# Kernel tuning notes

Measured on AMD Instinct MI355X. Metric: run time of the kernel, lower is better.

## Reference

```python
import jax, jax.numpy as jnp
import numpy as np

LN_EPS = 1e-9

def _layer_norm(x, g, b):
    mu = jnp.mean(x, axis=-1, keepdims=True)
    var = jnp.mean((x - mu) ** 2, axis=-1, keepdims=True)
    return (x - mu) * jax.lax.rsqrt(var + LN_EPS) * g + b

def _ffn(x, w1, b1, w2, b2, ln_g, ln_b):
    h = jax.nn.gelu(x @ w1 + b1, approximate=False)
    h = h @ w2 + b2
    return _layer_norm(h, ln_g, ln_b)

def _kernel_mean(x, y):
    d = x.shape[1]
    x2 = jnp.sum(x * x, axis=1)[:, None]
    y2 = jnp.sum(y * y, axis=1)[None, :]
    sq = x2 + y2 - 2.0 * (x @ y.T)  # [Nx, Ny]
    return jnp.mean(jnp.exp(-sq / (d * d)))

def _mmd(x, y):
    return _kernel_mean(x, x) + _kernel_mean(y, y) - 2.0 * _kernel_mean(x, y)

def setup_inputs() -> dict:
    key = jax.random.key(0)
    ks = jax.random.split(key, 8)
    B, S, D, DI, DL = 8, 512, 1024, 4096, 64
    s = lambda fan: 1.0 / np.sqrt(fan)
    return {
        "hidden": jax.random.normal(ks[0], (B, S, D), jnp.float32),
        "true_samples": jax.random.normal(ks[1], (B * S, DL), jnp.float32),
        "enc_w1": jax.random.normal(ks[2], (D, DI), jnp.float32) * s(D),
        "enc_b1": jnp.zeros((DI,), jnp.float32),
        "enc_w2": jax.random.normal(ks[3], (DI, DL), jnp.float32) * s(DI),
        "enc_b2": jnp.zeros((DL,), jnp.float32),
        "enc_ln_g": jnp.ones((DL,), jnp.float32),
        "enc_ln_b": jnp.zeros((DL,), jnp.float32),
        "dec_w1": jax.random.normal(ks[4], (DL, DI), jnp.float32) * s(DL),
        "dec_b1": jnp.zeros((DI,), jnp.float32),
        "dec_w2": jax.random.normal(ks[5], (DI, D), jnp.float32) * s(DI),
        "dec_b2": jnp.zeros((D,), jnp.float32),
        "dec_ln_g": jnp.ones((D,), jnp.float32),
        "dec_ln_b": jnp.zeros((D,), jnp.float32),
    }

def reference(hidden, true_samples, enc_w1, enc_b1, enc_w2, enc_b2, enc_ln_g, enc_ln_b,
              dec_w1, dec_b1, dec_w2, dec_b2, dec_ln_g, dec_ln_b):
    latent = _ffn(hidden, enc_w1, enc_b1, enc_w2, enc_b2, enc_ln_g, enc_ln_b)  # [B,S,DL]
    recon = _ffn(latent, dec_w1, dec_b1, dec_w2, dec_b2, dec_ln_g, dec_ln_b)   # [B,S,D]
    B, S, DL = latent.shape
    lat_flat = latent.reshape(-1, DL)  # [B*S, DL]
    reg_loss = _mmd(true_samples, lat_flat) / B * S
    return recon, latent, reg_loss
```

## Files before the change

### kernel.cpp

```cpp
#include <hip/hip_runtime.h>
#include <hip/hip_bf16.h>
#include <math.h>


typedef __attribute__((ext_vector_type(8))) short short8;
typedef __attribute__((ext_vector_type(4))) float float4a;
typedef __attribute__((ext_vector_type(4))) unsigned short us4;

__device__ inline ushort bf16r(float x) {
    union { float f; unsigned u; } c; c.f = x;
    unsigned r = (c.u + 0x7fffu + ((c.u >> 16) & 1u)) >> 16;
    return (ushort)r;
}

__device__ inline void gld_lds16(const void* g, void* l) {
    __builtin_amdgcn_global_load_lds(
        (const __attribute__((address_space(1))) void*)g,
        (__attribute__((address_space(3))) void*)l, 16, 0, 0);
}

template <int N> __device__ inline void wait_vmcnt() {
    if constexpr (N == 0) asm volatile("s_waitcnt vmcnt(0)" ::: "memory");
    else if constexpr (N == 4) asm volatile("s_waitcnt vmcnt(4)" ::: "memory");
    else if constexpr (N == 6) asm volatile("s_waitcnt vmcnt(6)" ::: "memory");
}

template <int N> __device__ inline void wait_lgkmcnt() {
    if constexpr (N == 0) asm volatile("s_waitcnt lgkmcnt(0)" ::: "memory");
    else if constexpr (N == 2) asm volatile("s_waitcnt lgkmcnt(2)" ::: "memory");
    else if constexpr (N == 4) asm volatile("s_waitcnt lgkmcnt(4)" ::: "memory");
    else if constexpr (N == 6) asm volatile("s_waitcnt lgkmcnt(6)" ::: "memory");
    else if constexpr (N == 8) asm volatile("s_waitcnt lgkmcnt(8)" ::: "memory");
    else if constexpr (N == 12) asm volatile("s_waitcnt lgkmcnt(12)" ::: "memory");
}

__device__ inline void wait_lgkm_dyn(int n) {
    if (n == 0) wait_lgkmcnt<0>();
    else if (n == 2) wait_lgkmcnt<2>();
    else if (n == 4) wait_lgkmcnt<4>();
    else if (n == 6) wait_lgkmcnt<6>();
    else wait_lgkmcnt<8>();
}

__device__ inline float fast_gelu(float v) {
    float v2 = v * v;
    float u = v * __builtin_fmaf(0.07135481627f, v2, 1.5957691216f);
    u = fminf(u, 30.0f);
    float e = __expf(u);
    return v * e * __builtin_amdgcn_rcpf(e + 1.0f);
}

__global__ __launch_bounds__(256) void k_pre(
        const float* __restrict__ hidden, ushort* __restrict__ A1bf,
        const float* __restrict__ tsamp, ushort* __restrict__ Tbf,
        float* __restrict__ sq_t, float* __restrict__ acc,
        const float* __restrict__ i0, ushort* __restrict__ o0,
        const float* __restrict__ i1, ushort* __restrict__ o1,
        const float* __restrict__ i2, ushort* __restrict__ o2,
        const float* __restrict__ i3, ushort* __restrict__ o3) {
    int b = blockIdx.x, tid = threadIdx.x;
    if (b == 0 && tid < 24) acc[tid] = 0.0f;
    if (b < 4096) {
        int i = b * 1024 + tid * 4;
        float4 v = *(const float4*)(hidden + i);
        us4 o = {bf16r(v.x), bf16r(v.y), bf16r(v.z), bf16r(v.w)};
        *(us4*)(A1bf + i) = o;
        return;
    }
    if (b < 4352) {
        int i = (b - 4096) * 1024 + tid * 4;
        float4 v = *(const float4*)(tsamp + i);
        us4 o = {bf16r(v.x), bf16r(v.y), bf16r(v.z), bf16r(v.w)};
        *(us4*)(Tbf + i) = o;
        float s = v.x * v.x + v.y * v.y + v.z * v.z + v.w * v.w;
#pragma unroll
        for (int off = 8; off; off >>= 1) s += __shfl_xor(s, off);
        if ((tid & 15) == 0) sq_t[i >> 6] = s;
        return;
    }
    __shared__ float t[32][65];
    const float* in; ushort* out; int R, C;
    int lb = b - 4352;
    if (lb < 2048)      { in = i0; out = o0; R = 1024; C = 4096; }
    else if (lb < 2176) { in = i1; out = o1; R = 4096; C = 64;   lb -= 2048; }
    else if (lb < 2304) { in = i2; out = o2; R = 64;   C = 4096; lb -= 2176; }
    else                { in = i3; out = o3; R = 4096; C = 1024; lb -= 2304; }
    int bx = (lb % (C / 32)) * 32;
    int by = (lb / (C / 32)) * 64;
    int tx = tid & 31, ty = tid >> 5;
#pragma unroll
    for (int i = 0; i < 64; i += 8)
        t[tx][i + ty] = in[(size_t)(by + i + ty) * C + (bx + tx)];
    __syncthreads();
#pragma unroll
    for (int i = 0; i < 32; i += 8) {
        int c = i + ty;
        ushort2 o;
        o.x = bf16r(t[c][2 * tx]);
        o.y = bf16r(t[c][2 * tx + 1]);
        *(ushort2*)(&out[(size_t)(bx + c) * R + by + 2 * tx]) = o;
    }
}

template <int BN, int EPI, bool SWZ>
__global__ __launch_bounds__(256) void k_gemm(
        const ushort* __restrict__ A, const ushort* __restrict__ Bt,
        const float* __restrict__ bias, void* __restrict__ Out,
        float* __restrict__ Out2, int M, int N, int K, int KC) {
    constexpr int BM = 128, BK = 64;
    constexpr int WAVES_N = BN / 64;
    constexpr int WAVES_M = 4 / WAVES_N;
    constexpr int WM = BM / WAVES_M;
    constexpr int MT = WM / 16;
    constexpr int NT = 4;
    constexpr int CA = BM / 32, CB = BN / 32;

    __shared__ ushort sA[BM * 64];
    __shared__ ushort sB[BN * 64];

    const int tid  = threadIdx.x;
    const int wave = tid >> 6, lane = tid & 63;
    const int wm = wave / WAVES_N, wn = wave % WAVES_N;
    int bx = blockIdx.x, by = blockIdx.y;
    if constexpr (SWZ) {
        int lin = blockIdx.x + gridDim.x * blockIdx.y;
        by = lin % gridDim.y;
        bx = lin / gridDim.y;
    }
    const int m0 = by * BM, n0 = bx * BN;
    const int lrow = lane & 15, lq = lane >> 4;
    const int srow8 = lane >> 3;
    const int sk8   = lane & 7;
    const int kbeg = blockIdx.z * KC;

    const ushort* pA[CA]; unsigned lA[CA];
#pragma unroll
    for (int j = 0; j < CA; ++j) {
        int c = wave * CA + j;
        int r = c * 8 + srow8;
        pA[j] = &A[(size_t)(m0 + r) * K + kbeg + ((sk8 ^ (r & 7)) * 8)];
        lA[j] = c * 512;
    }
    const ushort* pB[CB]; unsigned lB[CB];
#pragma unroll
    for (int j = 0; j < CB; ++j) {
        int c = wave * CB + j;
        int r = c * 8 + srow8;
        pB[j] = &Bt[(size_t)(n0 + r) * K + kbeg + ((sk8 ^ (r & 7)) * 8)];
        lB[j] = c * 512;
    }
    unsigned aoff[2][MT], boff[2][NT];
#pragma unroll
    for (int h = 0; h < 2; ++h) {
#pragma unroll
        for (int mt = 0; mt < MT; ++mt) {
            int r = wm * WM + mt * 16 + lrow;
            aoff[h][mt] = r * 64 + (((h * 4 + lq) ^ (r & 7)) * 8);
        }
#pragma unroll
        for (int nt = 0; nt < NT; ++nt) {
            int r = wn * 64 + nt * 16 + lrow;
            boff[h][nt] = r * 64 + (((h * 4 + lq) ^ (r & 7)) * 8);
        }
    }

    float4a acc[MT][NT];
#pragma unroll
    for (int mt = 0; mt < MT; ++mt)
#pragma unroll
        for (int nt = 0; nt < NT; ++nt)
            acc[mt][nt] = (float4a){0.f, 0.f, 0.f, 0.f};

    for (int k0 = 0; k0 < KC; k0 += BK) {
#pragma unroll
        for (int j = 0; j < CA; ++j) {
            gld_lds16(pA[j], &sA[lA[j]]);
            pA[j] += BK;
        }
#pragma unroll
        for (int j = 0; j < CB; ++j) {
            gld_lds16(pB[j], &sB[lB[j]]);
            pB[j] += BK;
        }
        __syncthreads();
#pragma unroll
        for (int h = 0; h < 2; ++h) {
            short8 af[MT], bfr[NT];
#pragma unroll
            for (int mt = 0; mt < MT; ++mt)
                af[mt] = *(short8*)(&sA[aoff[h][mt]]);
#pragma unroll
            for (int nt = 0; nt < NT; ++nt)
                bfr[nt] = *(short8*)(&sB[boff[h][nt]]);
#pragma unroll
            for (int mt = 0; mt < MT; ++mt)
#pragma unroll
                for (int nt = 0; nt < NT; ++nt)
                    acc[mt][nt] = __builtin_amdgcn_mfma_f32_16x16x32_bf16(
                        af[mt], bfr[nt], acc[mt][nt], 0, 0, 0);
        }
        __syncthreads();
    }

    float* dstp = nullptr;
    if constexpr (EPI == 2) {
        if (Out2 && blockIdx.z) dstp = Out2;
        else dstp = (float*)Out + (size_t)blockIdx.z * M * N;
    }
#pragma unroll
    for (int mt = 0; mt < MT; ++mt)
#pragma unroll
        for (int nt = 0; nt < NT; ++nt) {
            int col = n0 + wn * 64 + nt * 16 + lrow;
            float bv = 0.f;
            if constexpr (EPI != 2) bv = bias[col];
#pragma unroll
            for (int r = 0; r < 4; ++r) {
                int row = m0 + wm * WM + mt * 16 + lq * 4 + r;
                float v = acc[mt][nt][r] + bv;
                if constexpr (EPI == 0) {
                    ((ushort*)Out)[(size_t)row * N + col] = bf16r(fast_gelu(v));
                } else if constexpr (EPI == 1) {
                    ((float*)Out)[(size_t)row * N + col] = v;
                } else {
                    dstp[(size_t)row * N + col] = v;
                }
            }
        }
}

template <int BN, int EPI, int CX, int CY>
__global__ __launch_bounds__(512, 2) void k_gemm256mb(
        const ushort* __restrict__ A, const ushort* __restrict__ Bt,
        const float* __restrict__ bias, void* __restrict__ Out,
        float* __restrict__ Out2, int M, int N, int K, int KC) {
    constexpr int BM = 256, BK = 64;
    constexpr int AI = 4;
    constexpr int BI = BN / 64;
    constexpr int WAVES_N = BN / 64;
    constexpr int WAVES_M = 8 / WAVES_N;
    constexpr int WM = BM / WAVES_M;
    constexpr int MT = WM / 16;
    constexpr int NT = 4;

    __shared__ ushort sA[2][BM * 64];
    __shared__ ushort sB[2][BN * 64];

    const int tid = threadIdx.x;
    const int wave = tid >> 6, lane = tid & 63;
    const int wm = wave / WAVES_N, wn = wave % WAVES_N;

    const int gx = gridDim.x, gy = gridDim.y;
    const int lin = blockIdx.x + gx * (blockIdx.y + gy * blockIdx.z);
    const int nwg = gx * gy * gridDim.z;
    const int cpx = nwg >> 3;
    const int swz = (lin & 7) * cpx + (lin >> 3);
    const int nz  = gx * gy;
    const int zz  = swz / nz;
    const int rr  = swz % nz;
    const int chunk = rr / (CX * CY);
    const int lcl   = rr % (CX * CY);
    const int ncx   = gx / CX;
    const int bx = (chunk % ncx) * CX + (lcl % CX);
    const int by = (chunk / ncx) * CY + (lcl / CX);

    const int m0 = by * BM, n0 = bx * BN;
    const int lrow = lane & 15, lq = lane >> 4;
    const int kbeg = zz * KC;
    const int nT = KC / BK;

    const int crow = tid >> 3;
    const int ck8  = (tid & 7) ^ (crow & 7);
    const ushort* pAbase = A  + (size_t)(m0 + crow) * K + kbeg + ck8 * 8;
    const ushort* pBbase = Bt + (size_t)(n0 + crow) * K + kbeg + ck8 * 8;

    const int a0  = (wm * WM + lrow) * 64;
    const int b0  = (wn * 64 + lrow) * 64;
    const int sw0 = ((lq) ^ (lrow & 7)) * 8;
    const int sw1 = ((4 + lq) ^ (lrow & 7)) * 8;

    float4a acc[MT][NT];
#pragma unroll
    for (int mt = 0; mt < MT; ++mt)
#pragma unroll
        for (int nt = 0; nt < NT; ++nt)
            acc[mt][nt] = (float4a){0.f, 0.f, 0.f, 0.f};

#pragma unroll
    for (int j = 0; j < AI; ++j)
        gld_lds16(pAbase + (size_t)j * 64 * K, &sA[0][j * 4096 + wave * 512]);
#pragma unroll
    for (int j = 0; j < BI; ++j)
        gld_lds16(pBbase + (size_t)j * 64 * K, &sB[0][j * 4096 + wave * 512]);
    wait_vmcnt<0>();
    __builtin_amdgcn_s_barrier();
    __builtin_amdgcn_sched_barrier(0);

    for (int t = 0; t < nT; ++t) {
        const int d = t & 1;
        const bool pf1 = (t + 1 < nT);
        const size_t koff1 = (size_t)(t + 1) * BK;

        short8 af0[MT], bfr0[NT], af1[MT], bfr1[NT];
#pragma unroll
        for (int mt = 0; mt < MT; ++mt)
            af0[mt] = *(const short8*)(&sA[d][a0 + mt * 1024 + sw0]);
#pragma unroll
        for (int nt = 0; nt < NT; ++nt)
            bfr0[nt] = *(const short8*)(&sB[d][b0 + nt * 1024 + sw0]);
        __builtin_amdgcn_sched_barrier(0);
#pragma unroll
        for (int mt = 0; mt < MT; ++mt)
            af1[mt] = *(const short8*)(&sA[d][a0 + mt * 1024 + sw1]);
#pragma unroll
        for (int nt = 0; nt < NT; ++nt)
            bfr1[nt] = *(const short8*)(&sB[d][b0 + nt * 1024 + sw1]);
        if (pf1) {
#pragma unroll
            for (int j = 0; j < AI; ++j)
                gld_lds16(pAbase + (size_t)j * 64 * K + koff1,
                          &sA[d ^ 1][j * 4096 + wave * 512]);
#pragma unroll
            for (int j = 0; j < BI; ++j)
                gld_lds16(pBbase + (size_t)j * 64 * K + koff1,
                          &sB[d ^ 1][j * 4096 + wave * 512]);
        }
        wait_lgkmcnt<MT + 4>();
        __builtin_amdgcn_sched_barrier(0);
        __builtin_amdgcn_s_setprio(1);
#pragma unroll
        for (int mt = 0; mt < MT; ++mt)
#pragma unroll
            for (int nt = 0; nt < NT; ++nt)
                acc[mt][nt] = __builtin_amdgcn_mfma_f32_16x16x32_bf16(
                    af0[mt], bfr0[nt], acc[mt][nt], 0, 0, 0);
        __builtin_amdgcn_s_setprio(0);
        wait_lgkmcnt<0>();
        __builtin_amdgcn_sched_barrier(0);
        __builtin_amdgcn_s_setprio(1);
#pragma unroll
        for (int mt = 0; mt < MT; ++mt)
#pragma unroll
            for (int nt = 0; nt < NT; ++nt)
                acc[mt][nt] = __builtin_amdgcn_mfma_f32_16x16x32_bf16(
                    af1[mt], bfr1[nt], acc[mt][nt], 0, 0, 0);
        __builtin_amdgcn_s_setprio(0);
        if (pf1) {
            wait_vmcnt<0>();
            __builtin_amdgcn_s_barrier();
            __builtin_amdgcn_sched_barrier(0);
        }
    }

    float* dstp = nullptr;
    if constexpr (EPI == 2) {
        if (Out2 && zz) dstp = Out2;
        else dstp = (float*)Out + (size_t)zz * M * N;
    }
#pragma unroll
    for (int mt = 0; mt < MT; ++mt)
#pragma unroll
        for (int nt = 0; nt < NT; ++nt) {
            const int col = n0 + wn * 64 + nt * 16 + lrow;
            float bv = 0.f;
            if constexpr (EPI == 0) bv = bias[col];
#pragma unroll
            for (int r = 0; r < 4; ++r) {
                const int row = m0 + wm * WM + mt * 16 + lq * 4 + r;
                float v = acc[mt][nt][r] + bv;
                if constexpr (EPI == 0)
                    ((ushort*)Out)[(size_t)row * N + col] = bf16r(fast_gelu(v));
                else
                    dstp[(size_t)row * N + col] = v;
            }
        }
}

template <int BN, int EPI, int CX, int CY>
__global__ __launch_bounds__(512, 2) void k_gemm256sp(
        const ushort* __restrict__ A, const ushort* __restrict__ Bt,
        const float* __restrict__ bias, void* __restrict__ Out,
        float* __restrict__ Out2, int M, int N, int K, int KC) {
    constexpr int BM = 256, BK = 64;
    constexpr int AI = 4;
    constexpr int BI = BN / 64;
    constexpr int WAVES_N = BN / 64;
    constexpr int WAVES_M = 8 / WAVES_N;
    constexpr int WM = BM / WAVES_M;
    constexpr int MT = WM / 16;
    constexpr int NT = 4;
    constexpr int NS = MT;
    constexpr int NS2 = MT / 2;

    __shared__ ushort sA[2][BM * 64];
    __shared__ ushort sB[2][BN * 64];

    const int tid = threadIdx.x;
    const int wave = tid >> 6, lane = tid & 63;
    const int wm = wave / WAVES_N, wn = wave % WAVES_N;

    const int gx = gridDim.x, gy = gridDim.y;
    const int lin = blockIdx.x + gx * (blockIdx.y + gy * blockIdx.z);
    const int nwg = gx * gy * gridDim.z;
    const int cpx = nwg >> 3;
    const int swz = (lin & 7) * cpx + (lin >> 3);
    const int nz  = gx * gy;
    const int zz  = swz / nz;
    const int rr  = swz % nz;
    const int chunk = rr / (CX * CY);
    const int lcl   = rr % (CX * CY);
    const int ncx   = gx / CX;
    const int bx = (chunk % ncx) * CX + (lcl % CX);
    const int by = (chunk / ncx) * CY + (lcl / CX);

    const int m0 = by * BM, n0 = bx * BN;
    const int lrow = lane & 15, lq = lane >> 4;
    const int kbeg = zz * KC;
    const int nT = KC / BK;

    const int crow = tid >> 3;
    const int ck8  = (tid & 7) ^ (crow & 7);
    const ushort* pAbase = A  + (size_t)(m0 + crow) * K + kbeg + ck8 * 8;
    const ushort* pBbase = Bt + (size_t)(n0 + crow) * K + kbeg + ck8 * 8;

    const int a0  = (wm * WM + lrow) * 64;
    const int b0  = (wn * 64 + lrow) * 64;
    const int sw0 = ((lq) ^ (lrow & 7)) * 8;
    const int sw1 = ((4 + lq) ^ (lrow & 7)) * 8;

    float4a acc[MT][NT];
#pragma unroll
    for (int mt = 0; mt < MT; ++mt)
#pragma unroll
        for (int nt = 0; nt < NT; ++nt)
            acc[mt][nt] = (float4a){0.f, 0.f, 0.f, 0.f};

#pragma unroll
    for (int j = 0; j < AI; ++j)
        gld_lds16(pAbase + (size_t)j * 64 * K, &sA[0][j * 4096 + wave * 512]);
#pragma unroll
    for (int j = 0; j < BI; ++j)
        gld_lds16(pBbase + (size_t)j * 64 * K, &sB[0][j * 4096 + wave * 512]);
    wait_vmcnt<0>();
    __builtin_amdgcn_s_barrier();
    __builtin_amdgcn_sched_barrier(0);

    for (int t = 0; t < nT; ++t) {
        const int d = t & 1;
        const bool pf1 = (t + 1 < nT);
        const size_t koff1 = (size_t)(t + 1) * BK;

        short8 af[NS][2], bfr[2][NT];

#pragma unroll
        for (int nt = 0; nt < NT; ++nt)
            bfr[0][nt] = *(const short8*)(&sB[d][b0 + nt * 1024 + sw0]);
        af[0][0] = *(const short8*)(&sA[d][a0 + 0 * 1024 + sw0]);
        af[0][1] = *(const short8*)(&sA[d][a0 + 1 * 1024 + sw0]);
        __builtin_amdgcn_sched_barrier(0);
        af[1][0] = *(const short8*)(&sA[d][a0 + 2 * 1024 + sw0]);
        af[1][1] = *(const short8*)(&sA[d][a0 + 3 * 1024 + sw0]);
        __builtin_amdgcn_sched_barrier(0);
        if (pf1) {
#pragma unroll
            for (int j = 0; j < AI; ++j)
                gld_lds16(pAbase + (size_t)j * 64 * K + koff1,
                          &sA[d ^ 1][j * 4096 + wave * 512]);
#pragma unroll
            for (int j = 0; j < BI; ++j)
                gld_lds16(pBbase + (size_t)j * 64 * K + koff1,
                          &sB[d ^ 1][j * 4096 + wave * 512]);
        }
        __builtin_amdgcn_sched_barrier(0);

#pragma unroll
        for (int s = 0; s < NS; ++s) {
            const int s2 = s + 2;
            if (s2 < NS) {
                const int h2 = s2 / NS2;
                const int mb2 = (s2 % NS2) * 2;
                const int swh2 = h2 ? sw1 : sw0;
                if ((s2 % NS2) == 0) {
#pragma unroll
                    for (int nt = 0; nt < NT; ++nt)
                        bfr[h2][nt] =
                            *(const short8*)(&sB[d][b0 + nt * 1024 + swh2]);
                }
                af[s2][0] = *(const short8*)(&sA[d][a0 + (mb2 + 0) * 1024 + swh2]);
                af[s2][1] = *(const short8*)(&sA[d][a0 + (mb2 + 1) * 1024 + swh2]);
                __builtin_amdgcn_sched_barrier(0);
            }
            int Ns = 0;
            if (s + 1 < NS) Ns += (((s + 1) % NS2) == 0) ? (2 + NT) : 2;
            if (s + 2 < NS) Ns += (((s + 2) % NS2) == 0) ? (2 + NT) : 2;
            wait_lgkm_dyn(Ns);
            __builtin_amdgcn_sched_barrier(0);
            const int h = s / NS2, mb = (s % NS2) * 2;
            __builtin_amdgcn_s_setprio(1);
#pragma unroll
            for (int i = 0; i < 2; ++i)
#pragma unroll
                for (int nt = 0; nt < NT; ++nt)
                    acc[mb + i][nt] = __builtin_amdgcn_mfma_f32_16x16x32_bf16(
                        af[s][i], bfr[h][nt], acc[mb + i][nt], 0, 0, 0);
            __builtin_amdgcn_s_setprio(0);
        }
        if (pf1) {
            wait_vmcnt<0>();
            __builtin_amdgcn_s_barrier();
            __builtin_amdgcn_sched_barrier(0);
        }
    }

    float* dstp = nullptr;
    if constexpr (EPI == 2) {
        if (Out2 && zz) dstp = Out2;
        else dstp = (float*)Out + (size_t)zz * M * N;
    }
#pragma unroll
    for (int mt = 0; mt < MT; ++mt)
#pragma unroll
        for (int nt = 0; nt < NT; ++nt) {
            const int col = n0 + wn * 64 + nt * 16 + lrow;
            float bv = 0.f;
            if constexpr (EPI == 0) bv = bias[col];
#pragma unroll
            for (int r = 0; r < 4; ++r) {
                const int row = m0 + wm * WM + mt * 16 + lq * 4 + r;
                float v = acc[mt][nt][r] + bv;
                if constexpr (EPI == 0)
                    ((ushort*)Out)[(size_t)row * N + col] = bf16r(fast_gelu(v));
                else
                    dstp[(size_t)row * N + col] = v;
            }
        }
}

__global__ __launch_bounds__(256) void k_gram_all(
        const ushort* __restrict__ Tbf, const ushort* __restrict__ Lbf,
        const float* __restrict__ sq_t, const float* __restrict__ sq_l,
        float* __restrict__ accum) {
    __shared__ ushort sX[128 * 64];
    __shared__ ushort sY[128 * 64];
    __shared__ float red[4];

    int id = blockIdx.x;
    int pair, tbx, tby; float w;
    if (id < 1056) {
        pair = (id < 528) ? 0 : 1;
        int t = (pair == 0) ? id : id - 528;
        int r = (int)((sqrtf(8.0f * t + 1.0f) - 1.0f) * 0.5f);
        while ((r + 1) * (r + 2) / 2 <= t) ++r;
        while (r * (r + 1) / 2 > t) --r;
        tby = r; tbx = t - r * (r + 1) / 2;
        w = (tbx == tby) ? 1.0f : 2.0f;
    } else {
        pair = 2; int t = id - 1056;
        tbx = t & 31; tby = t >> 5; w = 1.0f;
    }
    const ushort* Xb = (pair == 1) ? Lbf : Tbf;
    const ushort* Yb = (pair == 0) ? Tbf : Lbf;
    const float* sqX = (pair == 1) ? sq_l : sq_t;
    const float* sqY = (pair == 0) ? sq_t : sq_l;

    const int tid  = threadIdx.x;
    const int wave = tid >> 6, lane = tid & 63;
    const int wm = wave >> 1, wn = wave & 1;
    const int bx = tbx * 128, by = tby * 128;
    const int lrow = lane & 15, lq = lane >> 4;
    const int srow8 = lane >> 3, sk8 = lane & 7;

#pragma unroll
    for (int j = 0; j < 4; ++j) {
        int c = wave * 4 + j;
        int r = c * 8 + srow8;
        int kc = (sk8 ^ (r & 7)) * 8;
        gld_lds16(&Xb[(size_t)(bx + r) * 64 + kc], &sX[c * 512]);
        gld_lds16(&Yb[(size_t)(by + r) * 64 + kc], &sY[c * 512]);
    }

    unsigned xoff[2][4], yoff[2][4];
#pragma unroll
    for (int h = 0; h < 2; ++h)
#pragma unroll
        for (int i = 0; i < 4; ++i) {
            int rx = wm * 64 + i * 16 + lrow;
            int ry = wn * 64 + i * 16 + lrow;
            xoff[h][i] = rx * 64 + (((h * 4 + lq) ^ (rx & 7)) * 8);
            yoff[h][i] = ry * 64 + (((h * 4 + lq) ^ (ry & 7)) * 8);
        }
    __syncthreads();

    float4a acc[4][4];
#pragma unroll
    for (int mt = 0; mt < 4; ++mt)
#pragma unroll
        for (int nt = 0; nt < 4; ++nt)
            acc[mt][nt] = (float4a){0.f, 0.f, 0.f, 0.f};

#pragma unroll
    for (int h = 0; h < 2; ++h) {
        short8 xf[4], yf[4];
#pragma unroll
        for (int mt = 0; mt < 4; ++mt)
            xf[mt] = *(short8*)(&sX[xoff[h][mt]]);
#pragma unroll
        for (int nt = 0; nt < 4; ++nt)
            yf[nt] = *(short8*)(&sY[yoff[h][nt]]);
#pragma unroll
        for (int mt = 0; mt < 4; ++mt)
#pragma unroll
            for (int nt = 0; nt < 4; ++nt)
                acc[mt][nt] = __builtin_amdgcn_mfma_f32_16x16x32_bf16(
                    xf[mt], yf[nt], acc[mt][nt], 0, 0, 0);
    }

    float sy[4];
#pragma unroll
    for (int nt = 0; nt < 4; ++nt)
        sy[nt] = sqY[by + wn * 64 + nt * 16 + lrow];
    float s = 0.f;
#pragma unroll
    for (int mt = 0; mt < 4; ++mt)
#pragma unroll
        for (int r = 0; r < 4; ++r) {
            float sx = sqX[bx + wm * 64 + mt * 16 + lq * 4 + r];
#pragma unroll
            for (int nt = 0; nt < 4; ++nt)
                s += __expf((2.0f * acc[mt][nt][r] - sx - sy[nt]) * (1.0f / 4096.0f));
        }
    s *= w;
#pragma unroll
    for (int off = 32; off; off >>= 1) s += __shfl_xor(s, off);
    if ((tid & 63) == 0) red[tid >> 6] = s;
    __syncthreads();
    if (tid == 0) atomicAdd(accum + pair * 8, red[0] + red[1] + red[2] + red[3]);
}

__global__ __launch_bounds__(256) void k_ln64_red(
        const float* __restrict__ part, int npart,
        const float* __restrict__ bias, const float* __restrict__ g,
        const float* __restrict__ b, float* __restrict__ outf,
        ushort* __restrict__ outb, float* __restrict__ sq_l) {
    int wave = threadIdx.x >> 6, lane = threadIdx.x & 63;
    int row = blockIdx.x * 4 + wave;
    float x = bias[lane];
    for (int s = 0; s < npart; ++s)
        x += part[(size_t)s * 4096 * 64 + row * 64 + lane];
    float s = x;
#pragma unroll
    for (int off = 32; off; off >>= 1) s += __shfl_xor(s, off);
    float mu = s * (1.0f / 64.0f);
    float d = x - mu;
    float v = d * d;
#pragma unroll
    for (int off = 32; off; off >>= 1) v += __shfl_xor(v, off);
    float rs = rsqrtf(v * (1.0f / 64.0f) + 1e-9f);
    float y = d * rs * g[lane] + b[lane];
    outf[row * 64 + lane] = y;
    outb[row * 64 + lane] = bf16r(y);
    float q = y * y;
#pragma unroll
    for (int off = 32; off; off >>= 1) q += __shfl_xor(q, off);
    if (lane == 0) sq_l[row] = q;
}

__global__ __launch_bounds__(256) void k_ln1024_red(
        const float* __restrict__ p0, const float* __restrict__ p1,
        const float* __restrict__ bias, const float* __restrict__ g,
        const float* __restrict__ b, float* __restrict__ out) {
    __shared__ float red[4];
    int row = blockIdx.x, tid = threadIdx.x;
    const float4 v0 = *(const float4*)(p0 + (size_t)row * 1024 + tid * 4);
    const float4 v1 = *(const float4*)(p1 + (size_t)row * 1024 + tid * 4);
    const float4 bb = *(const float4*)(bias + tid * 4);
    float4 v;
    v.x = v0.x + v1.x + bb.x;
    v.y = v0.y + v1.y + bb.y;
    v.z = v0.z + v1.z + bb.z;
    v.w = v0.w + v1.w + bb.w;
    float s = v.x + v.y + v.z + v.w;
#pragma unroll
    for (int off = 32; off; off >>= 1) s += __shfl_xor(s, off);
    if ((tid & 63) == 0) red[tid >> 6] = s;
    __syncthreads();
    float mu = (red[0] + red[1] + red[2] + red[3]) * (1.0f / 1024.0f);
    float dx = v.x - mu, dy = v.y - mu, dz = v.z - mu, dw = v.w - mu;
    float q = dx * dx + dy * dy + dz * dz + dw * dw;
#pragma unroll
    for (int off = 32; off; off >>= 1) q += __shfl_xor(q, off);
    __syncthreads();
    if ((tid & 63) == 0) red[tid >> 6] = q;
    __syncthreads();
    float rs = rsqrtf((red[0] + red[1] + red[2] + red[3]) * (1.0f / 1024.0f) + 1e-9f);
    const float4 gv = *(const float4*)(g + tid * 4);
    const float4 bv = *(const float4*)(b + tid * 4);
    float4 o;
    o.x = dx * rs * gv.x + bv.x;
    o.y = dy * rs * gv.y + bv.y;
    o.z = dz * rs * gv.z + bv.z;
    o.w = dw * rs * gv.w + bv.w;
    *(float4*)(out + (size_t)row * 1024 + tid * 4) = o;
}

__global__ void k_finalize(const float* __restrict__ accum, float* __restrict__ out) {
    out[0] = (accum[0] + accum[8] - 2.0f * accum[16]) * (64.0f / (4096.0f * 4096.0f));
}

extern "C" void kernel_launch(void* const* d_in, const int* in_sizes, int n_in,
                              void* d_out, int out_size, void* d_ws, size_t ws_size,
                              hipStream_t stream) {
    const float* hidden   = (const float*)d_in[0];
    const float* tsamp    = (const float*)d_in[1];
    const float* enc_w1   = (const float*)d_in[2];
    const float* enc_b1   = (const float*)d_in[3];
    const float* enc_w2   = (const float*)d_in[4];
    const float* enc_b2   = (const float*)d_in[5];
    const float* enc_ln_g = (const float*)d_in[6];
    const float* enc_ln_b = (const float*)d_in[7];
    const float* dec_w1   = (const float*)d_in[8];
    const float* dec_b1   = (const float*)d_in[9];
    const float* dec_w2   = (const float*)d_in[10];
    const float* dec_b2   = (const float*)d_in[11];
    const float* dec_ln_g = (const float*)d_in[12];
    const float* dec_ln_b = (const float*)d_in[13];

    float* out      = (float*)d_out;
    float* recon    = out;
    float* latent_f = out + 4194304;
    float* reg      = out + 4456448;

    char* ws = (char*)d_ws;
    const size_t MB = 1024 * 1024;
    ushort* A1bf = (ushort*)(ws + 0);
    ushort* W1t  = (ushort*)(ws + 8 * MB);
    float*  part = (float*)(ws + 0);
    float*  h4p0 = (float*)(ws + 0);
    ushort* H1bf = (ushort*)(ws + 16 * MB);
    ushort* W4t  = (ushort*)(ws + 48 * MB);
    ushort* W2t  = (ushort*)(ws + 56 * MB);
    ushort* W3t  = (ushort*)(ws + 56 * MB + 512 * 1024);
    ushort* Lbf  = (ushort*)(ws + 57 * MB);
    float*  sq_t = (float*)(ws + 59 * MB);
    float*  sq_l = (float*)(ws + 59 * MB + 16384);
    float*  acc3 = (float*)(ws + 59 * MB + 32768);
    ushort* Tbf  = (ushort*)(ws + 59 * MB + 65536);

    k_pre<<<8704, 256, 0, stream>>>(hidden, A1bf, tsamp, Tbf, sq_t, acc3,
                                    enc_w1, W1t, enc_w2, W2t,
                                    dec_w1, W3t, dec_w2, W4t);

    k_gemm256mb<256, 0, 4, 8><<<dim3(16, 16, 1), 512, 0, stream>>>(
        A1bf, W1t, enc_b1, H1bf, nullptr, 4096, 4096, 1024, 1024);
    k_gemm<64, 2, false><<<dim3(1, 32, 16), 256, 0, stream>>>(
        H1bf, W2t, nullptr, part, nullptr, 4096, 64, 4096, 256);
    k_ln64_red<<<1024, 256, 0, stream>>>(part, 16, enc_b2, enc_ln_g, enc_ln_b,
                                         latent_f, Lbf, sq_l);

    k_gemm<64, 0, false><<<dim3(64, 32, 1), 256, 0, stream>>>(
        Lbf, W3t, dec_b1, H1bf, nullptr, 4096, 4096, 64, 64);
    k_gemm256sp<128, 2, 8, 4><<<dim3(8, 16, 2), 512, 0, stream>>>(
        H1bf, W4t, nullptr, h4p0, recon, 4096, 1024, 4096, 2048);
    k_ln1024_red<<<4096, 256, 0, stream>>>(h4p0, recon, dec_b2, dec_ln_g,
                                           dec_ln_b, recon);

    k_gram_all<<<2080, 256, 0, stream>>>(Tbf, Lbf, sq_t, sq_l, acc3);
    k_finalize<<<1, 1, 0, stream>>>(acc3, reg);
}
```

Measured before the change: 270.1 us.

## Fuse encoder FFN second GEMM into first GEMM epilogue via LDS-staged activations

The encoder's first GEMM (4096x4096x1024 with GELU) now stages its bf16 GELU tile in LDS and immediately multiplies it by the matching 256-row slice of W2t. Each N-block writes a partial 4096x64 latent sum that the existing LN reduction combines. This removes the H1 write/readback and a separate split-K GEMM launch. The decoder's second GEMM switches from the split-phase variant to the existing k_gemm256mb template, and the main loop uses a simpler two-half LDS prefetch schedule. The cost is an extra LDS round trip, barriers, and uncached global loads of W2 in the epilogue.

```diff
diff --git a/kernel.cpp b/kernel.cpp
--- a/kernel.cpp
+++ b/kernel.cpp
@@ -32,14 +32,6 @@
     else if constexpr (N == 6) asm volatile("s_waitcnt lgkmcnt(6)" ::: "memory");
     else if constexpr (N == 8) asm volatile("s_waitcnt lgkmcnt(8)" ::: "memory");
     else if constexpr (N == 12) asm volatile("s_waitcnt lgkmcnt(12)" ::: "memory");
-}
-
-__device__ inline void wait_lgkm_dyn(int n) {
-    if (n == 0) wait_lgkmcnt<0>();
-    else if (n == 2) wait_lgkmcnt<2>();
-    else if (n == 4) wait_lgkmcnt<4>();
-    else if (n == 6) wait_lgkmcnt<6>();
-    else wait_lgkmcnt<8>();
 }
 
 __device__ inline float fast_gelu(float v) {
@@ -376,52 +368,41 @@
         }
 }
 
-template <int BN, int EPI, int CX, int CY>
-__global__ __launch_bounds__(512, 2) void k_gemm256sp(
+__global__ __launch_bounds__(512, 2) void k_gemm1f(
         const ushort* __restrict__ A, const ushort* __restrict__ Bt,
-        const float* __restrict__ bias, void* __restrict__ Out,
-        float* __restrict__ Out2, int M, int N, int K, int KC) {
-    constexpr int BM = 256, BK = 64;
-    constexpr int AI = 4;
-    constexpr int BI = BN / 64;
-    constexpr int WAVES_N = BN / 64;
-    constexpr int WAVES_M = 8 / WAVES_N;
-    constexpr int WM = BM / WAVES_M;
-    constexpr int MT = WM / 16;
-    constexpr int NT = 4;
-    constexpr int NS = MT;
-    constexpr int NS2 = MT / 2;
-
-    __shared__ ushort sA[2][BM * 64];
-    __shared__ ushort sB[2][BN * 64];
+        const float* __restrict__ bias, const ushort* __restrict__ W2t,
+        float* __restrict__ part, int M, int N, int K) {
+    constexpr int BM = 256, BN = 256, BK = 64;
+    constexpr int AI = 4, BI = 4;
+    constexpr int WAVES_N = 4;
+    constexpr int WM = 128;
+    constexpr int MT = 8, NT = 4;
+    constexpr int CX = 4, CY = 8;
+
+    __shared__ ushort smem[65536];
 
     const int tid = threadIdx.x;
     const int wave = tid >> 6, lane = tid & 63;
     const int wm = wave / WAVES_N, wn = wave % WAVES_N;
 
     const int gx = gridDim.x, gy = gridDim.y;
-    const int lin = blockIdx.x + gx * (blockIdx.y + gy * blockIdx.z);
-    const int nwg = gx * gy * gridDim.z;
-    const int cpx = nwg >> 3;
+    const int lin = blockIdx.x + gx * blockIdx.y;
+    const int cpx = (gx * gy) >> 3;
     const int swz = (lin & 7) * cpx + (lin >> 3);
-    const int nz  = gx * gy;
-    const int zz  = swz / nz;
-    const int rr  = swz % nz;
-    const int chunk = rr / (CX * CY);
-    const int lcl   = rr % (CX * CY);
+    const int chunk = swz / (CX * CY);
+    const int lcl   = swz % (CX * CY);
     const int ncx   = gx / CX;
     const int bx = (chunk % ncx) * CX + (lcl % CX);
     const int by = (chunk / ncx) * CY + (lcl / CX);
 
     const int m0 = by * BM, n0 = bx * BN;
     const int lrow = lane & 15, lq = lane >> 4;
-    const int kbeg = zz * KC;
-    const int nT = KC / BK;
+    const int nT = K / BK;
 
     const int crow = tid >> 3;
     const int ck8  = (tid & 7) ^ (crow & 7);
-    const ushort* pAbase = A  + (size_t)(m0 + crow) * K + kbeg + ck8 * 8;
-    const ushort* pBbase = Bt + (size_t)(n0 + crow) * K + kbeg + ck8 * 8;
+    const ushort* pAbase = A  + (size_t)(m0 + crow) * K + ck8 * 8;
+    const ushort* pBbase = Bt + (size_t)(n0 + crow) * K + ck8 * 8;
 
     const int a0  = (wm * WM + lrow) * 64;
     const int b0  = (wn * 64 + lrow) * 64;
@@ -437,10 +418,11 @@
 
 #pragma unroll
     for (int j = 0; j < AI; ++j)
-        gld_lds16(pAbase + (size_t)j * 64 * K, &sA[0][j * 4096 + wave * 512]);
+        gld_lds16(pAbase + (size_t)j * 64 * K, &smem[j * 4096 + wave * 512]);
 #pragma unroll
     for (int j = 0; j < BI; ++j)
-        gld_lds16(pBbase + (size_t)j * 64 * K, &sB[0][j * 4096 + wave * 512]);
+        gld_lds16(pBbase + (size_t)j * 64 * K,
+                  &smem[32768 + j * 4096 + wave * 512]);
     wait_vmcnt<0>();
     __builtin_amdgcn_s_barrier();
     __builtin_amdgcn_sched_barrier(0);
@@ -449,62 +431,53 @@
         const int d = t & 1;
         const bool pf1 = (t + 1 < nT);
         const size_t koff1 = (size_t)(t + 1) * BK;
-
-        short8 af[NS][2], bfr[2][NT];
-
+        const ushort* sAd = &smem[d * 16384];
+        const ushort* sBd = &smem[32768 + d * 16384];
+
+        short8 af0[MT], bfr0[NT], af1[MT], bfr1[NT];
+#pragma unroll
+        for (int mt = 0; mt < MT; ++mt)
+            af0[mt] = *(const short8*)(&sAd[a0 + mt * 1024 + sw0]);
 #pragma unroll
         for (int nt = 0; nt < NT; ++nt)
-            bfr[0][nt] = *(const short8*)(&sB[d][b0 + nt * 1024 + sw0]);
-        af[0][0] = *(const short8*)(&sA[d][a0 + 0 * 1024 + sw0]);
-        af[0][1] = *(const short8*)(&sA[d][a0 + 1 * 1024 + sw0]);
+            bfr0[nt] = *(const short8*)(&sBd[b0 + nt * 1024 + sw0]);
         __builtin_amdgcn_sched_barrier(0);
-        af[1][0] = *(const short8*)(&sA[d][a0 + 2 * 1024 + sw0]);
-        af[1][1] = *(const short8*)(&sA[d][a0 + 3 * 1024 + sw0]);
-        __builtin_amdgcn_sched_barrier(0);
+#pragma unroll
+        for (int mt = 0; mt < MT; ++mt)
+            af1[mt] = *(const short8*)(&sAd[a0 + mt * 1024 + sw1]);
+#pragma unroll
+        for (int nt = 0; nt < NT; ++nt)
+            bfr1[nt] = *(const short8*)(&sBd[b0 + nt * 1024 + sw1]);
         if (pf1) {
 #pragma unroll
             for (int j = 0; j < AI; ++j)
                 gld_lds16(pAbase + (size_t)j * 64 * K + koff1,
-                          &sA[d ^ 1][j * 4096 + wave * 512]);
+                          &smem[(d ^ 1) * 16384 + j * 4096 + wave * 512]);
 #pragma unroll
             for (int j = 0; j < BI; ++j)
                 gld_lds16(pBbase + (size_t)j * 64 * K + koff1,
-                          &sB[d ^ 1][j * 4096 + wave * 512]);
-        }
+                          &smem[32768 + (d ^ 1) * 16384 + j * 4096 + wave * 512]);
+        }
+        wait_lgkmcnt<12>();
         __builtin_amdgcn_sched_barrier(0);
-
-#pragma unroll
-        for (int s = 0; s < NS; ++s) {
-            const int s2 = s + 2;
-            if (s2 < NS) {
-                const int h2 = s2 / NS2;
-                const int mb2 = (s2 % NS2) * 2;
-                const int swh2 = h2 ? sw1 : sw0;
-                if ((s2 % NS2) == 0) {
-#pragma unroll
-                    for (int nt = 0; nt < NT; ++nt)
-                        bfr[h2][nt] =
-                            *(const short8*)(&sB[d][b0 + nt * 1024 + swh2]);
-                }
-                af[s2][0] = *(const short8*)(&sA[d][a0 + (mb2 + 0) * 1024 + swh2]);
-                af[s2][1] = *(const short8*)(&sA[d][a0 + (mb2 + 1) * 1024 + swh2]);
-                __builtin_amdgcn_sched_barrier(0);
-            }
-            int Ns = 0;
-            if (s + 1 < NS) Ns += (((s + 1) % NS2) == 0) ? (2 + NT) : 2;
-            if (s + 2 < NS) Ns += (((s + 2) % NS2) == 0) ? (2 + NT) : 2;
-            wait_lgkm_dyn(Ns);
-            __builtin_amdgcn_sched_barrier(0);
-            const int h = s / NS2, mb = (s % NS2) * 2;
-            __builtin_amdgcn_s_setprio(1);
-#pragma unroll
-            for (int i = 0; i < 2; ++i)
-#pragma unroll
-                for (int nt = 0; nt < NT; ++nt)
-                    acc[mb + i][nt] = __builtin_amdgcn_mfma_f32_16x16x32_bf16(
-                        af[s][i], bfr[h][nt], acc[mb + i][nt], 0, 0, 0);
-            __builtin_amdgcn_s_setprio(0);
-        }
+        __builtin_amdgcn_s_setprio(1);
+#pragma unroll
+        for (int mt = 0; mt < MT; ++mt)
+#pragma unroll
+            for (int nt = 0; nt < NT; ++nt)
+                acc[mt][nt] = __builtin_amdgcn_mfma_f32_16x16x32_bf16(
+                    af0[mt], bfr0[nt], acc[mt][nt], 0, 0, 0);
+        __builtin_amdgcn_s_setprio(0);
+        wait_lgkmcnt<0>();
+        __builtin_amdgcn_sched_barrier(0);
+        __builtin_amdgcn_s_setprio(1);
+#pragma unroll
+        for (int mt = 0; mt < MT; ++mt)
+#pragma unroll
+            for (int nt = 0; nt < NT; ++nt)
+                acc[mt][nt] = __builtin_amdgcn_mfma_f32_16x16x32_bf16(
+                    af1[mt], bfr1[nt], acc[mt][nt], 0, 0, 0);
+        __builtin_amdgcn_s_setprio(0);
         if (pf1) {
             wait_vmcnt<0>();
             __builtin_amdgcn_s_barrier();
@@ -512,26 +485,65 @@
         }
     }
 
-    float* dstp = nullptr;
-    if constexpr (EPI == 2) {
-        if (Out2 && zz) dstp = Out2;
-        else dstp = (float*)Out + (size_t)zz * M * N;
-    }
+    __syncthreads();
 #pragma unroll
     for (int mt = 0; mt < MT; ++mt)
 #pragma unroll
         for (int nt = 0; nt < NT; ++nt) {
-            const int col = n0 + wn * 64 + nt * 16 + lrow;
-            float bv = 0.f;
-            if constexpr (EPI == 0) bv = bias[col];
-#pragma unroll
-            for (int r = 0; r < 4; ++r) {
-                const int row = m0 + wm * WM + mt * 16 + lq * 4 + r;
-                float v = acc[mt][nt][r] + bv;
-                if constexpr (EPI == 0)
-                    ((ushort*)Out)[(size_t)row * N + col] = bf16r(fast_gelu(v));
-                else
-                    dstp[(size_t)row * N + col] = v;
+            const int c = wn * 64 + nt * 16 + lrow;
+            const float bv = bias[n0 + c];
+            const int s = c >> 3, cl = c & 7;
+#pragma unroll
+            for (int r_ = 0; r_ < 4; ++r_) {
+                const int r = wm * WM + mt * 16 + lq * 4 + r_;
+                const int sz = (s & 24) | ((s & 7) ^ (r & 7));
+                smem[r * 256 + sz * 8 + cl] =
+                    bf16r(fast_gelu(acc[mt][nt][r_] + bv));
+            }
+        }
+    __syncthreads();
+
+    float4a pacc[2][4];
+#pragma unroll
+    for (int m2 = 0; m2 < 2; ++m2)
+#pragma unroll
+        for (int n2 = 0; n2 < 4; ++n2)
+            pacc[m2][n2] = (float4a){0.f, 0.f, 0.f, 0.f};
+
+    const ushort* gW2 = W2t + n0;
+#pragma unroll
+    for (int kk = 0; kk < 8; ++kk) {
+        short8 af2[2], bf2[4];
+#pragma unroll
+        for (int m2 = 0; m2 < 2; ++m2) {
+            const int r2 = wave * 32 + m2 * 16 + lrow;
+            const int s2 = kk * 4 + lq;
+            const int sz2 = (s2 & 24) | ((s2 & 7) ^ (r2 & 7));
+            af2[m2] = *(const short8*)(&smem[r2 * 256 + sz2 * 8]);
+        }
+#pragma unroll
+        for (int n2 = 0; n2 < 4; ++n2) {
+            const int l = n2 * 16 + lrow;
+            bf2[n2] = *(const short8*)(&gW2[(size_t)l * 4096 + kk * 32 + lq * 8]);
+        }
+#pragma unroll
+        for (int m2 = 0; m2 < 2; ++m2)
+#pragma unroll
+            for (int n2 = 0; n2 < 4; ++n2)
+                pacc[m2][n2] = __builtin_amdgcn_mfma_f32_16x16x32_bf16(
+                    af2[m2], bf2[n2], pacc[m2][n2], 0, 0, 0);
+    }
+
+    float* pz = part + (size_t)bx * M * 64;
+#pragma unroll
+    for (int m2 = 0; m2 < 2; ++m2)
+#pragma unroll
+        for (int n2 = 0; n2 < 4; ++n2) {
+            const int lat = n2 * 16 + lrow;
+#pragma unroll
+            for (int r_ = 0; r_ < 4; ++r_) {
+                const int row = m0 + wave * 32 + m2 * 16 + lq * 4 + r_;
+                pz[(size_t)row * 64 + lat] = pacc[m2][n2][r_];
             }
         }
 }
@@ -734,9 +746,9 @@
     const size_t MB = 1024 * 1024;
     ushort* A1bf = (ushort*)(ws + 0);
     ushort* W1t  = (ushort*)(ws + 8 * MB);
-    float*  part = (float*)(ws + 0);
     float*  h4p0 = (float*)(ws + 0);
     ushort* H1bf = (ushort*)(ws + 16 * MB);
+    float*  part = (float*)(ws + 16 * MB);
     ushort* W4t  = (ushort*)(ws + 48 * MB);
     ushort* W2t  = (ushort*)(ws + 56 * MB);
     ushort* W3t  = (ushort*)(ws + 56 * MB + 512 * 1024);
@@ -750,16 +762,14 @@
                                     enc_w1, W1t, enc_w2, W2t,
                                     dec_w1, W3t, dec_w2, W4t);
 
-    k_gemm256mb<256, 0, 4, 8><<<dim3(16, 16, 1), 512, 0, stream>>>(
-        A1bf, W1t, enc_b1, H1bf, nullptr, 4096, 4096, 1024, 1024);
-    k_gemm<64, 2, false><<<dim3(1, 32, 16), 256, 0, stream>>>(
-        H1bf, W2t, nullptr, part, nullptr, 4096, 64, 4096, 256);
+    k_gemm1f<<<dim3(16, 16, 1), 512, 0, stream>>>(
+        A1bf, W1t, enc_b1, W2t, part, 4096, 4096, 1024);
     k_ln64_red<<<1024, 256, 0, stream>>>(part, 16, enc_b2, enc_ln_g, enc_ln_b,
                                          latent_f, Lbf, sq_l);
 
     k_gemm<64, 0, false><<<dim3(64, 32, 1), 256, 0, stream>>>(
         Lbf, W3t, dec_b1, H1bf, nullptr, 4096, 4096, 64, 64);
-    k_gemm256sp<128, 2, 8, 4><<<dim3(8, 16, 2), 512, 0, stream>>>(
+    k_gemm256mb<128, 2, 8, 4><<<dim3(8, 16, 2), 512, 0, stream>>>(
         H1bf, W4t, nullptr, h4p0, recon, 4096, 1024, 4096, 2048);
     k_ln1024_red<<<4096, 256, 0, stream>>>(h4p0, recon, dec_b2, dec_ln_g,
                                            dec_ln_b, recon);
```

Measured after the change: 260.6 us. 3.5% less time.
